# Optimization experiments

Hardware: AMD Instinct MI355X
Metric: run time of the kernel (lower is better)

Reference implementation:

```python
import jax, jax.numpy as jnp
import numpy as np

EMBED = 512
HEADS = 64
DK = EMBED // HEADS  # == n_wires_attn == 8
NW_FFN = 8
FFN = 2048
EPS = 1e-5


def _layernorm(x, g, b):
    mu = jnp.mean(x, axis=-1, keepdims=True)
    var = jnp.var(x, axis=-1, keepdims=True)
    return (x - mu) * jax.lax.rsqrt(var + EPS) * g + b


def setup_inputs() -> dict:
    key = jax.random.key(0)
    ks = jax.random.split(key, 12)
    d = {
        "x": jax.random.normal(ks[0], (4, 1024, EMBED), dtype=jnp.float32),
        # attention quantum RX params (one per wire, shared across heads/tokens)
        "phi": jax.random.normal(ks[1], (DK,), dtype=jnp.float32) * 0.1,
        # combine_heads linear
        "Wc": jax.random.normal(ks[2], (EMBED, EMBED), dtype=jnp.float32) / np.sqrt(EMBED),
        "bc": jnp.zeros((EMBED,), dtype=jnp.float32),
        # FFN quantum RY params
        "theta": jax.random.normal(ks[3], (NW_FFN,), dtype=jnp.float32) * 0.1,
        "W1": jax.random.normal(ks[4], (NW_FFN, FFN), dtype=jnp.float32) / np.sqrt(NW_FFN),
        "b1": jnp.zeros((FFN,), dtype=jnp.float32),
        "W2": jax.random.normal(ks[5], (FFN, EMBED), dtype=jnp.float32) / np.sqrt(FFN),
        "b2": jnp.zeros((EMBED,), dtype=jnp.float32),
        "g1": jnp.ones((EMBED,), dtype=jnp.float32),
        "be1": jnp.zeros((EMBED,), dtype=jnp.float32),
        "g2": jnp.ones((EMBED,), dtype=jnp.float32),
        "be2": jnp.zeros((EMBED,), dtype=jnp.float32),
    }
    return d


def reference(x, phi, Wc, bc, theta, W1, b1, W2, b2, g1, be1, g2, be2):
    B, S, E = x.shape
    # --- quantum attention projections ---
    # Per head-row of DK features: RX(x_i) encoder then trainable RX(phi_i),
    xh = x.reshape(B, S, HEADS, DK)
    qkv = jnp.cos(xh + phi)                     # [B,S,H,DK]
    qkv = jnp.transpose(qkv, (0, 2, 1, 3))      # [B,H,S,DK]
    scores = jnp.einsum('bhqd,bhkd->bhqk', qkv, qkv) / jnp.sqrt(jnp.float32(DK))
    attn = jax.nn.softmax(scores, axis=-1)
    out = jnp.einsum('bhqk,bhkd->bhqd', attn, qkv)
    out = jnp.transpose(out, (0, 2, 1, 3)).reshape(B, S, E)
    attn_out = out @ Wc.T if False else out @ Wc + bc  # combine_heads linear
    x1 = _layernorm(x + attn_out, g1, be1)
    # --- quantum FFN: RX(x_i) then trainable RY(theta_i) -> <Z> = cos(x_i)*cos(theta_i)
    qout = jnp.cos(x1[..., :NW_FFN]) * jnp.cos(theta)   # [B,S,NW_FFN]
    h = jax.nn.relu(qout @ W1 + b1)
    ffn_out = h @ W2 + b2
    return _layernorm(x1 + ffn_out, g2, be2)
```

## Files before the change

kernel.cpp:

```cpp
#include <hip/hip_runtime.h>
#include <hip/hip_bf16.h>
#include <math.h>

#define B 4
#define S 1024
#define E 512
#define H 64
#define DK 8
#define FFN 2048
#define BS (B*S)

#define CSCALE 0.7141879f

#if __has_builtin(__builtin_amdgcn_exp2f)
#define EXP2F(x) __builtin_amdgcn_exp2f(x)
#else
#define EXP2F(x) exp2f(x)
#endif

typedef __attribute__((ext_vector_type(8))) short short8;
typedef __attribute__((ext_vector_type(4))) float float4a;

union U8 { short8 v; unsigned u[4]; };
union F4 { float4a v; float f[4]; };

__device__ __forceinline__ unsigned short f2bf(float f) {
    unsigned u = __builtin_bit_cast(unsigned, f);
    u = (u + 0x7fffu + ((u >> 16) & 1u)) >> 16;
    return (unsigned short)u;
}
__device__ __forceinline__ float bf2f(unsigned short h) {
    return __builtin_bit_cast(float, (unsigned)h << 16);
}
__device__ __forceinline__ unsigned packbf(float a, float b) {
    return __builtin_amdgcn_perm(__builtin_bit_cast(unsigned, a),
                                 __builtin_bit_cast(unsigned, b), 0x07060302u);
}
__device__ __forceinline__ unsigned packbf_rn(float a, float b) {
    return ((unsigned)f2bf(a) << 16) | f2bf(b);
}
__device__ __forceinline__ int pidx(int k) {
    return (k & ~31) | (((k >> 2) & 3) << 3) | (((k >> 4) & 1) << 2) | (k & 3);
}

__device__ __forceinline__ void glds16(const void* g, void* l) {
    __builtin_amdgcn_global_load_lds(
        (const __attribute__((address_space(1))) void*)g,
        (__attribute__((address_space(3))) void*)l, 16, 0, 0);
}

__global__ __launch_bounds__(512) void attn_conv_kernel(const float* __restrict__ x,
                                                        const float* __restrict__ phi,
                                                        const float* __restrict__ Wc,
                                                        const float* __restrict__ W2,
                                                        const float* __restrict__ W1,
                                                        const float* __restrict__ b1,
                                                        unsigned short* __restrict__ Afrag,
                                                        unsigned short* __restrict__ W2f,
                                                        unsigned short* __restrict__ Wcf,
                                                        unsigned short* __restrict__ W1f) {
    __shared__ unsigned short kv[(S + 16) * DK];
    __shared__ unsigned short vtp[9][S + 8];
    int bid = blockIdx.x;
    int tid = threadIdx.x;
    const short8 z8 = {0,0,0,0,0,0,0,0};

    if (bid < 336) {
        int idx = bid * 512 + tid;
        if (idx < 131072) {
            int lane = idx & 63, c = idx >> 6;
            int ntile = c >> 6, kb32 = c & 63;
            int g = lane >> 4, col = lane & 15;
            int n = ntile * 16 + col, kb = kb32 * 32;
            short8 o;
            #pragma unroll
            for (int j = 0; j < 8; j++) {
                int k = kb + 16 * (j >> 2) + 4 * g + (j & 3);
                o[j] = (short)f2bf(W2[(size_t)k * 512 + n]);
            }
            *(short8*)&W2f[(size_t)idx * 8] = o;
        } else if (idx < 163840) {
            int i2 = idx - 131072;
            int lane = i2 & 63, c = i2 >> 6;
            int ntile = c >> 4, kb32 = c & 15;
            int g = lane >> 4, col = lane & 15;
            int n = ntile * 16 + col, kb = kb32 * 32;
            short8 o;
            #pragma unroll
            for (int j = 0; j < 8; j++)
                o[j] = (short)f2bf(Wc[(size_t)(kb + g * 8 + j) * 512 + n]);
            *(short8*)&Wcf[(size_t)i2 * 8] = o;
        } else {
            int i3 = idx - 163840;
            if (i3 < 2048) {
                short8 o;
                #pragma unroll
                for (int j = 0; j < 8; j++) o[j] = (short)f2bf(W1[j * FFN + i3]);
                *(short8*)&W1f[(size_t)i3 * 8] = o;
            } else if (i3 < 4096) {
                int f = i3 - 2048;
                short8 o = z8;
                o[0] = (short)f2bf(b1[f]);
                *(short8*)&W1f[(size_t)i3 * 8] = o;
            } else if (i3 < 4112) {
                *(short8*)&W1f[(size_t)i3 * 8] = z8;
            }
        }
        return;
    }

    int abid = bid - 336;
    int head = abid >> 2, qquad = abid & 3;
    int b = head >> 6, hh = head & 63;

    float ph[DK];
    #pragma unroll
    for (int d = 0; d < DK; d++) ph[d] = phi[d];

    {
        int r2 = tid * 2;
        unsigned short vb[8][2];
        #pragma unroll
        for (int j = 0; j < 2; j++) {
            const float* xp = x + ((size_t)(b * S + r2 + j)) * E + hh * DK;
            float4 u = *(const float4*)xp;
            float4 v = *(const float4*)(xp + 4);
            float c[8] = {__cosf(u.x+ph[0]), __cosf(u.y+ph[1]), __cosf(u.z+ph[2]), __cosf(u.w+ph[3]),
                          __cosf(v.x+ph[4]), __cosf(v.y+ph[5]), __cosf(v.z+ph[6]), __cosf(v.w+ph[7])};
            U8 kr;
            kr.u[0] = packbf_rn(c[1] * CSCALE, c[0] * CSCALE);
            kr.u[1] = packbf_rn(c[3] * CSCALE, c[2] * CSCALE);
            kr.u[2] = packbf_rn(c[5] * CSCALE, c[4] * CSCALE);
            kr.u[3] = packbf_rn(c[7] * CSCALE, c[6] * CSCALE);
            *(short8*)&kv[(r2 + j) * DK] = kr.v;
            #pragma unroll
            for (int d = 0; d < 8; d++) vb[d][j] = f2bf(c[d]);
        }
        int pr = pidx(r2);
        #pragma unroll
        for (int d = 0; d < 8; d++)
            *(unsigned*)&vtp[d][pr] = (unsigned)vb[d][0] | ((unsigned)vb[d][1] << 16);
        *(unsigned*)&vtp[8][pr] = 0x3F803F80u;
    }
    if (tid < 16) *(short8*)&kv[(S + tid) * DK] = z8;
    __syncthreads();

    int w = tid >> 6, lane = tid & 63, col = lane & 15, g = lane >> 4;
    bool g0 = (g == 0);
    int q0 = qquad * 256 + w * 32;
    const float4a zc = {0.f,0.f,0.f,0.f};

    short8 aq[2];
    #pragma unroll
    for (int t = 0; t < 2; t++)
        aq[t] = g0 ? *(const short8*)&kv[(q0 + t*16 + col) * DK] : z8;

    float4a acc[2];
    acc[0] = zc; acc[1] = zc;

    int vrow = col < 8 ? col : 8;
    const unsigned short* vbase = &vtp[vrow][0];

    int off0 = g0 ? col * DK : S * DK;
    int off1 = g0 ? (16 + col) * DK : S * DK;
    int stepo = g0 ? 32 * DK : 0;

    short8 bk0 = *(const short8*)&kv[off0];
    short8 bk1 = *(const short8*)&kv[off1];
    off0 += stepo; off1 += stepo;

    for (int kb = 0; kb < S; kb += 32) {
        __builtin_amdgcn_s_setprio(1);
        float4a s00 = __builtin_amdgcn_mfma_f32_16x16x32_bf16(bk0, aq[0], zc, 0,0,0);
        float4a s01 = __builtin_amdgcn_mfma_f32_16x16x32_bf16(bk1, aq[0], zc, 0,0,0);
        float4a s10 = __builtin_amdgcn_mfma_f32_16x16x32_bf16(bk0, aq[1], zc, 0,0,0);
        float4a s11 = __builtin_amdgcn_mfma_f32_16x16x32_bf16(bk1, aq[1], zc, 0,0,0);
        __builtin_amdgcn_s_setprio(0);
        short8 vf = *(const short8*)(vbase + kb + g * 8);
        short8 nbk0 = *(const short8*)&kv[off0];
        short8 nbk1 = *(const short8*)&kv[off1];
        off0 += stepo; off1 += stepo;
        F4 S00, S01, S10, S11;
        S00.v = s00; S01.v = s01; S10.v = s10; S11.v = s11;
        float ea0 = EXP2F(S00.f[0]);
        float ea1 = EXP2F(S00.f[1]);
        float ea2 = EXP2F(S00.f[2]);
        float ea3 = EXP2F(S00.f[3]);
        float eb0 = EXP2F(S01.f[0]);
        float eb1 = EXP2F(S01.f[1]);
        float eb2 = EXP2F(S01.f[2]);
        float eb3 = EXP2F(S01.f[3]);
        float ec0 = EXP2F(S10.f[0]);
        float ec1 = EXP2F(S10.f[1]);
        float ec2 = EXP2F(S10.f[2]);
        float ec3 = EXP2F(S10.f[3]);
        float ed0 = EXP2F(S11.f[0]);
        float ed1 = EXP2F(S11.f[1]);
        float ed2 = EXP2F(S11.f[2]);
        float ed3 = EXP2F(S11.f[3]);
        U8 pf0, pf1;
        pf0.u[0] = packbf(ea1, ea0);
        pf0.u[1] = packbf(ea3, ea2);
        pf0.u[2] = packbf(eb1, eb0);
        pf0.u[3] = packbf(eb3, eb2);
        pf1.u[0] = packbf(ec1, ec0);
        pf1.u[1] = packbf(ec3, ec2);
        pf1.u[2] = packbf(ed1, ed0);
        pf1.u[3] = packbf(ed3, ed2);
        __builtin_amdgcn_s_setprio(1);
        acc[0] = __builtin_amdgcn_mfma_f32_16x16x32_bf16(vf, pf0.v, acc[0], 0,0,0);
        acc[1] = __builtin_amdgcn_mfma_f32_16x16x32_bf16(vf, pf1.v, acc[1], 0,0,0);
        __builtin_amdgcn_s_setprio(0);
        bk0 = nbk0; bk1 = nbk1;
    }
    int lp8 = ((hh & 3) * 16 + col) * 8;
    #pragma unroll
    for (int t = 0; t < 2; t++) {
        F4 a; a.v = acc[t];
        float denom = __shfl(a.f[0], 32 + col);
        float inv = __builtin_amdgcn_rcpf(denom);
        if (g < 2) {
            int chunk = (hh >> 2) * 256 + (b * 64 + qquad * 16 + w * 2 + t);
            uint2 o;
            o.x = packbf_rn(a.f[1] * inv, a.f[0] * inv);
            o.y = packbf_rn(a.f[3] * inv, a.f[2] * inv);
            *(uint2*)&Afrag[(size_t)chunk * 512 + lp8 + g * 4] = o;
        }
    }
}

__global__ __launch_bounds__(512) void combine_ln1(const unsigned short* __restrict__ Afrag,
                                                   const unsigned short* __restrict__ Wcf,
                                                   const float* __restrict__ bc,
                                                   const float* __restrict__ x,
                                                   const float* __restrict__ g1,
                                                   const float* __restrict__ be1,
                                                   float* __restrict__ x1out,
                                                   unsigned short* __restrict__ qoutbf,
                                                   const float* __restrict__ theta) {
    __shared__ unsigned short As[16 * 64 * 8];
    __shared__ float xout[16][516];
    int tt = blockIdx.x;
    int tid = threadIdx.x;
    int w = tid >> 6, lane = tid & 63;
    int wbase = (tid & ~63) * 8;

    #pragma unroll
    for (int r = 0; r < 2; r++) {
        const unsigned short* gsrc =
            Afrag + ((size_t)((r * 8 + w) * 256 + tt) * 64 + lane) * 8;
        glds16(gsrc, &As[r * 4096 + wbase]);
    }
    asm volatile("s_waitcnt vmcnt(0)" ::: "memory");
    __syncthreads();

    int col = lane & 15, g = lane >> 4;
    const float4a zc = {0.f,0.f,0.f,0.f};
    float4a acc[4];
    #pragma unroll
    for (int nt = 0; nt < 4; nt++) acc[nt] = zc;

    const unsigned short* wp = Wcf + ((size_t)(w * 4096) + lane) * 8;

    short8 bfA[4], bfB[4];
    #pragma unroll
    for (int nt = 0; nt < 4; nt++)
        bfA[nt] = *(const short8*)(wp + nt * 8192);

    for (int kb32 = 0; kb32 < 16; kb32 += 2) {
        #pragma unroll
        for (int nt = 0; nt < 4; nt++)
            bfB[nt] = *(const short8*)(wp + nt * 8192 + (kb32 + 1) * 512);
        short8 af = *(const short8*)&As[(kb32 * 64 + lane) * 8];
        #pragma unroll
        for (int nt = 0; nt < 4; nt++)
            acc[nt] = __builtin_amdgcn_mfma_f32_16x16x32_bf16(af, bfA[nt], acc[nt], 0, 0, 0);
        if (kb32 + 2 < 16) {
            #pragma unroll
            for (int nt = 0; nt < 4; nt++)
                bfA[nt] = *(const short8*)(wp + nt * 8192 + (kb32 + 2) * 512);
        }
        af = *(const short8*)&As[((kb32 + 1) * 64 + lane) * 8];
        #pragma unroll
        for (int nt = 0; nt < 4; nt++)
            acc[nt] = __builtin_amdgcn_mfma_f32_16x16x32_bf16(af, bfB[nt], acc[nt], 0, 0, 0);
    }
    #pragma unroll
    for (int nt = 0; nt < 4; nt++) {
        int n = w * 64 + nt * 16 + col;
        float bb = bc[n];
        #pragma unroll
        for (int r = 0; r < 4; r++)
            xout[g * 4 + r][n] = acc[nt][r] + bb;
    }
    __syncthreads();

    int hl = lane >> 5, l = lane & 31;
    int token = w * 2 + hl;
    int e0 = l * 16;
    size_t grow = ((size_t)tt * 16 + token) * 512;
    float v[16];
    float s = 0.f, sq = 0.f;
    #pragma unroll
    for (int u = 0; u < 4; u++) {
        float4 xv = *(const float4*)&x[grow + e0 + u * 4];
        float4 pv = *(const float4*)&xout[token][e0 + u * 4];
        float a0 = xv.x + pv.x, a1 = xv.y + pv.y, a2 = xv.z + pv.z, a3 = xv.w + pv.w;
        v[u*4] = a0; v[u*4+1] = a1; v[u*4+2] = a2; v[u*4+3] = a3;
        s += a0 + a1 + a2 + a3;
        sq += a0*a0 + a1*a1 + a2*a2 + a3*a3;
    }
    #pragma unroll
    for (int off = 1; off <= 16; off <<= 1) {
        s  += __shfl_xor(s, off);
        sq += __shfl_xor(sq, off);
    }
    float mu = s * (1.f / 512.f);
    float var = sq * (1.f / 512.f) - mu * mu;
    float rstd = rsqrtf(var + 1e-5f);
    float y[16];
    #pragma unroll
    for (int u = 0; u < 4; u++) {
        float4 gv = *(const float4*)&g1[e0 + u * 4];
        float4 bv = *(const float4*)&be1[e0 + u * 4];
        y[u*4]   = (v[u*4]   - mu) * rstd * gv.x + bv.x;
        y[u*4+1] = (v[u*4+1] - mu) * rstd * gv.y + bv.y;
        y[u*4+2] = (v[u*4+2] - mu) * rstd * gv.z + bv.z;
        y[u*4+3] = (v[u*4+3] - mu) * rstd * gv.w + bv.w;
        float4 o = make_float4(y[u*4], y[u*4+1], y[u*4+2], y[u*4+3]);
        *(float4*)&x1out[grow + e0 + u * 4] = o;
    }
    if (l == 0) {
        U8 q;
        q.u[0] = packbf_rn(__cosf(y[1]) * __cosf(theta[1]), __cosf(y[0]) * __cosf(theta[0]));
        q.u[1] = packbf_rn(__cosf(y[3]) * __cosf(theta[3]), __cosf(y[2]) * __cosf(theta[2]));
        q.u[2] = packbf_rn(__cosf(y[5]) * __cosf(theta[5]), __cosf(y[4]) * __cosf(theta[4]));
        q.u[3] = packbf_rn(__cosf(y[7]) * __cosf(theta[7]), __cosf(y[6]) * __cosf(theta[6]));
        *(short8*)&qoutbf[((size_t)tt * 16 + token) * 8] = q.v;
    }
}

__global__ __launch_bounds__(256) void ffn_mfma(const unsigned short* __restrict__ qbf,
                                                const unsigned short* __restrict__ W1fg,
                                                const unsigned short* __restrict__ W2f,
                                                const float* __restrict__ b2,
                                                unsigned short* __restrict__ Cbf) {
    __shared__ float accs[2][64][36];
    int tid = threadIdx.x;
    int w = tid >> 6, lane = tid & 63, col = lane & 15, g = lane >> 4;
    int ngw = w & 1, kh = w >> 1;
    int tb = blockIdx.x >> 2, nb = blockIdx.x & 3;
    int mw = tb * 32;
    int ntile0 = nb * 8 + ngw * 4;
    int kb32b = kh * 32;
    const short8 z8 = {0,0,0,0,0,0,0,0};
    const short8 one8 = {(short)0x3F80,0,0,0,0,0,0,0};
    const float4a zc = {0.f,0.f,0.f,0.f};

    short8 qf[2];
    #pragma unroll
    for (int t = 0; t < 2; t++)
        qf[t] = (g == 0) ? *(const short8*)&qbf[(size_t)(mw + t * 16 + col) * 8]
                         : (g == 1 ? one8 : z8);

    float4a acc[2][4];
    #pragma unroll
    for (int t = 0; t < 2; t++)
        #pragma unroll
        for (int nt = 0; nt < 4; nt++) acc[t][nt] = zc;

    const unsigned short* w2p = W2f + (size_t)ntile0 * 64 * 512 + lane * 8;
    const unsigned short* w1p =
        (g == 0) ? W1fg + (size_t)(kb32b * 32 + col) * 8 :
        (g == 1) ? W1fg + 16384 + (size_t)(kb32b * 32 + col) * 8 :
                   W1fg + 32768;
    int w1step = (g < 2) ? 256 : 0;

    short8 afA[4], afB[4], w1A0, w1A1, w1B0, w1B1;
    #pragma unroll
    for (int nt = 0; nt < 4; nt++)
        afA[nt] = *(const short8*)(w2p + nt * 32768 + (size_t)kb32b * 512);
    w1A0 = *(const short8*)w1p;
    w1A1 = *(const short8*)(w1p + 128);
    w1p += w1step;

#define FFN_BODY(AF, W10, W11)                                                    \
    {                                                                             \
        _Pragma("unroll")                                                         \
        for (int t = 0; t < 2; t++) {                                             \
            float4a h0 = __builtin_amdgcn_mfma_f32_16x16x32_bf16(W10, qf[t], zc, 0,0,0); \
            float4a h1 = __builtin_amdgcn_mfma_f32_16x16x32_bf16(W11, qf[t], zc, 0,0,0); \
            F4 H0, H1; H0.v = h0; H1.v = h1;                                      \
            float e00 = fmaxf(H0.f[0], 0.f);                                      \
            float e01 = fmaxf(H0.f[1], 0.f);                                      \
            float e02 = fmaxf(H0.f[2], 0.f);                                      \
            float e03 = fmaxf(H0.f[3], 0.f);                                      \
            float e10 = fmaxf(H1.f[0], 0.f);                                      \
            float e11 = fmaxf(H1.f[1], 0.f);                                      \
            float e12 = fmaxf(H1.f[2], 0.f);                                      \
            float e13 = fmaxf(H1.f[3], 0.f);                                      \
            U8 pf;                                                                \
            pf.u[0] = packbf(e01, e00);                                           \
            pf.u[1] = packbf(e03, e02);                                           \
            pf.u[2] = packbf(e11, e10);                                           \
            pf.u[3] = packbf(e13, e12);                                           \
            _Pragma("unroll")                                                     \
            for (int nt = 0; nt < 4; nt++)                                        \
                acc[t][nt] = __builtin_amdgcn_mfma_f32_16x16x32_bf16(AF[nt], pf.v, \
                                                                     acc[t][nt], 0,0,0); \
        }                                                                         \
    }

    for (int i = 0; i < 32; i += 2) {
        int kb32 = kb32b + i;
        #pragma unroll
        for (int nt = 0; nt < 4; nt++)
            afB[nt] = *(const short8*)(w2p + nt * 32768 + (size_t)(kb32 + 1) * 512);
        w1B0 = *(const short8*)w1p;
        w1B1 = *(const short8*)(w1p + 128);
        w1p += w1step;
        FFN_BODY(afA, w1A0, w1A1)
        #pragma unroll
        for (int nt = 0; nt < 4; nt++)
            afA[nt] = *(const short8*)(w2p + nt * 32768 + (size_t)(kb32 + 2) * 512);
        w1A0 = *(const short8*)w1p;
        w1A1 = *(const short8*)(w1p + 128);
        w1p += w1step;
        FFN_BODY(afB, w1B0, w1B1)
    }
#undef FFN_BODY

    if (kh == 1) {
        #pragma unroll
        for (int t = 0; t < 2; t++)
            #pragma unroll
            for (int nt = 0; nt < 4; nt++)
                *(float4a*)&accs[ngw][lane][(t * 4 + nt) * 4] = acc[t][nt];
    }
    __syncthreads();
    if (kh == 0) {
        #pragma unroll
        for (int t = 0; t < 2; t++)
            #pragma unroll
            for (int nt = 0; nt < 4; nt++)
                acc[t][nt] = acc[t][nt] +
                    *(const float4a*)&accs[ngw][lane][(t * 4 + nt) * 4];
        int n0 = ntile0 * 16;
        #pragma unroll
        for (int nt = 0; nt < 4; nt++) {
            float4 bb = *(const float4*)&b2[n0 + nt * 16 + 4 * g];
            #pragma unroll
            for (int t = 0; t < 2; t++) {
                F4 a; a.v = acc[t][nt];
                uint2 o;
                o.x = packbf_rn(a.f[1] + bb.y, a.f[0] + bb.x);
                o.y = packbf_rn(a.f[3] + bb.w, a.f[2] + bb.z);
                *(uint2*)&Cbf[(size_t)(mw + t * 16 + col) * 512 + n0 + nt * 16 + 4 * g] = o;
            }
        }
    }
}

__global__ __launch_bounds__(256) void ln_kernel(const float* __restrict__ a,
                                                 const unsigned short* __restrict__ r,
                                                 const float* __restrict__ g,
                                                 const float* __restrict__ be,
                                                 float* __restrict__ out) {
    int t = blockIdx.x * 4 + (threadIdx.x >> 6);
    int lane = threadIdx.x & 63;
    size_t base = (size_t)t * E;
    int e0 = lane * 8;
    float4 a0 = *(const float4*)&a[base + e0];
    float4 a1 = *(const float4*)&a[base + e0 + 4];
    uint4 rv = *(const uint4*)&r[base + e0];
    float v[8];
    v[0] = a0.x + bf2f((unsigned short)(rv.x & 0xffff));
    v[1] = a0.y + bf2f((unsigned short)(rv.x >> 16));
    v[2] = a0.z + bf2f((unsigned short)(rv.y & 0xffff));
    v[3] = a0.w + bf2f((unsigned short)(rv.y >> 16));
    v[4] = a1.x + bf2f((unsigned short)(rv.z & 0xffff));
    v[5] = a1.y + bf2f((unsigned short)(rv.z >> 16));
    v[6] = a1.z + bf2f((unsigned short)(rv.w & 0xffff));
    v[7] = a1.w + bf2f((unsigned short)(rv.w >> 16));
    float s = 0.f, sq = 0.f;
    #pragma unroll
    for (int i = 0; i < 8; i++) { s += v[i]; sq += v[i] * v[i]; }
    #pragma unroll
    for (int off = 1; off <= 32; off <<= 1) {
        s  += __shfl_xor(s, off);
        sq += __shfl_xor(sq, off);
    }
    float mu = s * (1.f / E);
    float var = sq * (1.f / E) - mu * mu;
    float rstd = rsqrtf(var + 1e-5f);
    float4 g0 = *(const float4*)&g[e0];
    float4 g1v = *(const float4*)&g[e0 + 4];
    float4 b0 = *(const float4*)&be[e0];
    float4 b1v = *(const float4*)&be[e0 + 4];
    float4 o0, o1;
    o0.x = (v[0] - mu) * rstd * g0.x + b0.x;
    o0.y = (v[1] - mu) * rstd * g0.y + b0.y;
    o0.z = (v[2] - mu) * rstd * g0.z + b0.z;
    o0.w = (v[3] - mu) * rstd * g0.w + b0.w;
    o1.x = (v[4] - mu) * rstd * g1v.x + b1v.x;
    o1.y = (v[5] - mu) * rstd * g1v.y + b1v.y;
    o1.z = (v[6] - mu) * rstd * g1v.z + b1v.z;
    o1.w = (v[7] - mu) * rstd * g1v.w + b1v.w;
    *(float4*)&out[base + e0] = o0;
    *(float4*)&out[base + e0 + 4] = o1;
}

extern "C" void kernel_launch(void* const* d_in, const int* in_sizes, int n_in,
                              void* d_out, int out_size, void* d_ws, size_t ws_size,
                              hipStream_t stream) {
    const float* x     = (const float*)d_in[0];
    const float* phi   = (const float*)d_in[1];
    const float* Wc    = (const float*)d_in[2];
    const float* bc    = (const float*)d_in[3];
    const float* theta = (const float*)d_in[4];
    const float* W1    = (const float*)d_in[5];
    const float* b1    = (const float*)d_in[6];
    const float* W2    = (const float*)d_in[7];
    const float* b2    = (const float*)d_in[8];
    const float* g1    = (const float*)d_in[9];
    const float* be1   = (const float*)d_in[10];
    const float* g2    = (const float*)d_in[11];
    const float* be2   = (const float*)d_in[12];
    float* out = (float*)d_out;

    float* ws = (float*)d_ws;
    unsigned short* Afrag  = (unsigned short*)ws;
    unsigned short* W2f    = (unsigned short*)(ws + 1048576);
    unsigned short* Wcf    = (unsigned short*)(ws + 1572864);
    unsigned short* W1f    = (unsigned short*)(ws + 1703936);
    unsigned short* qoutbf = (unsigned short*)(ws + 1736704);

    attn_conv_kernel<<<1360, 512, 0, stream>>>(x, phi, Wc, W2, W1, b1,
                                               Afrag, W2f, Wcf, W1f);
    combine_ln1<<<256, 512, 0, stream>>>(Afrag, Wcf, bc, x, g1, be1,
                                         out, qoutbf, theta);
    ffn_mfma<<<512, 256, 0, stream>>>(qoutbf, W1f, W2f, b2, Afrag);
    ln_kernel<<<1024, 256, 0, stream>>>(out, Afrag, g2, be2, out);
}
```

Measured before the change: 155.7 us.

## Fuse FFN second GEMM with final residual LayerNorm in one kernel

Merges the FFN MFMA kernel and the separate LayerNorm kernel. Each 512-thread block now owns 16 full token rows across all 512 output columns with the full K range, and reduces the LayerNorm statistics through shared memory. This drops the bf16 intermediate write and read-back plus one launch, and removes the split-K shared-memory reduction. In exchange the FFN hidden activations for each 16-row tile are recomputed by every wave, W2 is re-streamed once per 16 rows instead of per 32, and the grid shrinks to 256 blocks. The final residual sum also stays in fp32 instead of being rounded to bf16.

Result: slower. 174.5 us (+12.1%).

```diff
diff --git a/kernel.cpp b/kernel.cpp
--- a/kernel.cpp
+++ b/kernel.cpp
@@ -340,79 +340,69 @@
     }
 }
 
-__global__ __launch_bounds__(256) void ffn_mfma(const unsigned short* __restrict__ qbf,
-                                                const unsigned short* __restrict__ W1fg,
-                                                const unsigned short* __restrict__ W2f,
-                                                const float* __restrict__ b2,
-                                                unsigned short* __restrict__ Cbf) {
-    __shared__ float accs[2][64][36];
+__global__ __launch_bounds__(512) void ffn_ln2(const unsigned short* __restrict__ qbf,
+                                               const unsigned short* __restrict__ W1fg,
+                                               const unsigned short* __restrict__ W2f,
+                                               const float* __restrict__ b2,
+                                               const float* __restrict__ g2,
+                                               const float* __restrict__ be2,
+                                               float* __restrict__ out) {
+    __shared__ float sums[8][16], sqs[8][16];
     int tid = threadIdx.x;
     int w = tid >> 6, lane = tid & 63, col = lane & 15, g = lane >> 4;
-    int ngw = w & 1, kh = w >> 1;
-    int tb = blockIdx.x >> 2, nb = blockIdx.x & 3;
-    int mw = tb * 32;
-    int ntile0 = nb * 8 + ngw * 4;
-    int kb32b = kh * 32;
+    int mw = blockIdx.x * 16;
+    int ntile0 = w * 4;
     const short8 z8 = {0,0,0,0,0,0,0,0};
     const short8 one8 = {(short)0x3F80,0,0,0,0,0,0,0};
     const float4a zc = {0.f,0.f,0.f,0.f};
 
-    short8 qf[2];
-    #pragma unroll
-    for (int t = 0; t < 2; t++)
-        qf[t] = (g == 0) ? *(const short8*)&qbf[(size_t)(mw + t * 16 + col) * 8]
+    short8 qf = (g == 0) ? *(const short8*)&qbf[(size_t)(mw + col) * 8]
                          : (g == 1 ? one8 : z8);
 
-    float4a acc[2][4];
-    #pragma unroll
-    for (int t = 0; t < 2; t++)
-        #pragma unroll
-        for (int nt = 0; nt < 4; nt++) acc[t][nt] = zc;
+    float4a acc[4];
+    #pragma unroll
+    for (int nt = 0; nt < 4; nt++) acc[nt] = zc;
 
     const unsigned short* w2p = W2f + (size_t)ntile0 * 64 * 512 + lane * 8;
     const unsigned short* w1p =
-        (g == 0) ? W1fg + (size_t)(kb32b * 32 + col) * 8 :
-        (g == 1) ? W1fg + 16384 + (size_t)(kb32b * 32 + col) * 8 :
+        (g == 0) ? W1fg + (size_t)col * 8 :
+        (g == 1) ? W1fg + 16384 + (size_t)col * 8 :
                    W1fg + 32768;
     int w1step = (g < 2) ? 256 : 0;
 
     short8 afA[4], afB[4], w1A0, w1A1, w1B0, w1B1;
     #pragma unroll
     for (int nt = 0; nt < 4; nt++)
-        afA[nt] = *(const short8*)(w2p + nt * 32768 + (size_t)kb32b * 512);
+        afA[nt] = *(const short8*)(w2p + nt * 32768);
     w1A0 = *(const short8*)w1p;
     w1A1 = *(const short8*)(w1p + 128);
     w1p += w1step;
 
 #define FFN_BODY(AF, W10, W11)                                                    \
     {                                                                             \
+        float4a h0 = __builtin_amdgcn_mfma_f32_16x16x32_bf16(W10, qf, zc, 0,0,0); \
+        float4a h1 = __builtin_amdgcn_mfma_f32_16x16x32_bf16(W11, qf, zc, 0,0,0); \
+        F4 H0, H1; H0.v = h0; H1.v = h1;                                          \
+        float e00 = fmaxf(H0.f[0], 0.f);                                          \
+        float e01 = fmaxf(H0.f[1], 0.f);                                          \
+        float e02 = fmaxf(H0.f[2], 0.f);                                          \
+        float e03 = fmaxf(H0.f[3], 0.f);                                          \
+        float e10 = fmaxf(H1.f[0], 0.f);                                          \
+        float e11 = fmaxf(H1.f[1], 0.f);                                          \
+        float e12 = fmaxf(H1.f[2], 0.f);                                          \
+        float e13 = fmaxf(H1.f[3], 0.f);                                          \
+        U8 pf;                                                                    \
+        pf.u[0] = packbf(e01, e00);                                               \
+        pf.u[1] = packbf(e03, e02);                                               \
+        pf.u[2] = packbf(e11, e10);                                               \
+        pf.u[3] = packbf(e13, e12);                                               \
         _Pragma("unroll")                                                         \
-        for (int t = 0; t < 2; t++) {                                             \
-            float4a h0 = __builtin_amdgcn_mfma_f32_16x16x32_bf16(W10, qf[t], zc, 0,0,0); \
-            float4a h1 = __builtin_amdgcn_mfma_f32_16x16x32_bf16(W11, qf[t], zc, 0,0,0); \
-            F4 H0, H1; H0.v = h0; H1.v = h1;                                      \
-            float e00 = fmaxf(H0.f[0], 0.f);                                      \
-            float e01 = fmaxf(H0.f[1], 0.f);                                      \
-            float e02 = fmaxf(H0.f[2], 0.f);                                      \
-            float e03 = fmaxf(H0.f[3], 0.f);                                      \
-            float e10 = fmaxf(H1.f[0], 0.f);                                      \
-            float e11 = fmaxf(H1.f[1], 0.f);                                      \
-            float e12 = fmaxf(H1.f[2], 0.f);                                      \
-            float e13 = fmaxf(H1.f[3], 0.f);                                      \
-            U8 pf;                                                                \
-            pf.u[0] = packbf(e01, e00);                                           \
-            pf.u[1] = packbf(e03, e02);                                           \
-            pf.u[2] = packbf(e11, e10);                                           \
-            pf.u[3] = packbf(e13, e12);                                           \
-            _Pragma("unroll")                                                     \
-            for (int nt = 0; nt < 4; nt++)                                        \
-                acc[t][nt] = __builtin_amdgcn_mfma_f32_16x16x32_bf16(AF[nt], pf.v, \
-                                                                     acc[t][nt], 0,0,0); \
-        }                                                                         \
-    }
-
-    for (int i = 0; i < 32; i += 2) {
-        int kb32 = kb32b + i;
+        for (int nt = 0; nt < 4; nt++)                                            \
+            acc[nt] = __builtin_amdgcn_mfma_f32_16x16x32_bf16(AF[nt], pf.v,       \
+                                                              acc[nt], 0,0,0);    \
+    }
+
+    for (int kb32 = 0; kb32 < 64; kb32 += 2) {
         #pragma unroll
         for (int nt = 0; nt < 4; nt++)
             afB[nt] = *(const short8*)(w2p + nt * 32768 + (size_t)(kb32 + 1) * 512);
@@ -430,84 +420,45 @@
     }
 #undef FFN_BODY
 
-    if (kh == 1) {
-        #pragma unroll
-        for (int t = 0; t < 2; t++)
-            #pragma unroll
-            for (int nt = 0; nt < 4; nt++)
-                *(float4a*)&accs[ngw][lane][(t * 4 + nt) * 4] = acc[t][nt];
-    }
+    int t = mw + col;
+    size_t base = (size_t)t * E;
+    int nb = w * 64 + 4 * g;
+    float v[16];
+    float s = 0.f, sq = 0.f;
+    #pragma unroll
+    for (int nt = 0; nt < 4; nt++) {
+        float4 bb = *(const float4*)&b2[nb + nt * 16];
+        float4 xv = *(const float4*)&out[base + nb + nt * 16];
+        F4 a; a.v = acc[nt];
+        float v0 = xv.x + a.f[0] + bb.x;
+        float v1 = xv.y + a.f[1] + bb.y;
+        float v2 = xv.z + a.f[2] + bb.z;
+        float v3 = xv.w + a.f[3] + bb.w;
+        v[nt*4] = v0; v[nt*4+1] = v1; v[nt*4+2] = v2; v[nt*4+3] = v3;
+        s += v0 + v1 + v2 + v3;
+        sq += v0*v0 + v1*v1 + v2*v2 + v3*v3;
+    }
+    s  += __shfl_xor(s, 16);  sq += __shfl_xor(sq, 16);
+    s  += __shfl_xor(s, 32);  sq += __shfl_xor(sq, 32);
+    if (lane < 16) { sums[w][col] = s; sqs[w][col] = sq; }
     __syncthreads();
-    if (kh == 0) {
-        #pragma unroll
-        for (int t = 0; t < 2; t++)
-            #pragma unroll
-            for (int nt = 0; nt < 4; nt++)
-                acc[t][nt] = acc[t][nt] +
-                    *(const float4a*)&accs[ngw][lane][(t * 4 + nt) * 4];
-        int n0 = ntile0 * 16;
-        #pragma unroll
-        for (int nt = 0; nt < 4; nt++) {
-            float4 bb = *(const float4*)&b2[n0 + nt * 16 + 4 * g];
-            #pragma unroll
-            for (int t = 0; t < 2; t++) {
-                F4 a; a.v = acc[t][nt];
-                uint2 o;
-                o.x = packbf_rn(a.f[1] + bb.y, a.f[0] + bb.x);
-                o.y = packbf_rn(a.f[3] + bb.w, a.f[2] + bb.z);
-                *(uint2*)&Cbf[(size_t)(mw + t * 16 + col) * 512 + n0 + nt * 16 + 4 * g] = o;
-            }
-        }
-    }
-}
-
-__global__ __launch_bounds__(256) void ln_kernel(const float* __restrict__ a,
-                                                 const unsigned short* __restrict__ r,
-                                                 const float* __restrict__ g,
-                                                 const float* __restrict__ be,
-                                                 float* __restrict__ out) {
-    int t = blockIdx.x * 4 + (threadIdx.x >> 6);
-    int lane = threadIdx.x & 63;
-    size_t base = (size_t)t * E;
-    int e0 = lane * 8;
-    float4 a0 = *(const float4*)&a[base + e0];
-    float4 a1 = *(const float4*)&a[base + e0 + 4];
-    uint4 rv = *(const uint4*)&r[base + e0];
-    float v[8];
-    v[0] = a0.x + bf2f((unsigned short)(rv.x & 0xffff));
-    v[1] = a0.y + bf2f((unsigned short)(rv.x >> 16));
-    v[2] = a0.z + bf2f((unsigned short)(rv.y & 0xffff));
-    v[3] = a0.w + bf2f((unsigned short)(rv.y >> 16));
-    v[4] = a1.x + bf2f((unsigned short)(rv.z & 0xffff));
-    v[5] = a1.y + bf2f((unsigned short)(rv.z >> 16));
-    v[6] = a1.z + bf2f((unsigned short)(rv.w & 0xffff));
-    v[7] = a1.w + bf2f((unsigned short)(rv.w >> 16));
-    float s = 0.f, sq = 0.f;
-    #pragma unroll
-    for (int i = 0; i < 8; i++) { s += v[i]; sq += v[i] * v[i]; }
-    #pragma unroll
-    for (int off = 1; off <= 32; off <<= 1) {
-        s  += __shfl_xor(s, off);
-        sq += __shfl_xor(sq, off);
-    }
-    float mu = s * (1.f / E);
-    float var = sq * (1.f / E) - mu * mu;
+    float SS = 0.f, QQ = 0.f;
+    #pragma unroll
+    for (int ww = 0; ww < 8; ww++) { SS += sums[ww][col]; QQ += sqs[ww][col]; }
+    float mu = SS * (1.f / E);
+    float var = QQ * (1.f / E) - mu * mu;
     float rstd = rsqrtf(var + 1e-5f);
-    float4 g0 = *(const float4*)&g[e0];
-    float4 g1v = *(const float4*)&g[e0 + 4];
-    float4 b0 = *(const float4*)&be[e0];
-    float4 b1v = *(const float4*)&be[e0 + 4];
-    float4 o0, o1;
-    o0.x = (v[0] - mu) * rstd * g0.x + b0.x;
-    o0.y = (v[1] - mu) * rstd * g0.y + b0.y;
-    o0.z = (v[2] - mu) * rstd * g0.z + b0.z;
-    o0.w = (v[3] - mu) * rstd * g0.w + b0.w;
-    o1.x = (v[4] - mu) * rstd * g1v.x + b1v.x;
-    o1.y = (v[5] - mu) * rstd * g1v.y + b1v.y;
-    o1.z = (v[6] - mu) * rstd * g1v.z + b1v.z;
-    o1.w = (v[7] - mu) * rstd * g1v.w + b1v.w;
-    *(float4*)&out[base + e0] = o0;
-    *(float4*)&out[base + e0 + 4] = o1;
+    #pragma unroll
+    for (int nt = 0; nt < 4; nt++) {
+        float4 gv = *(const float4*)&g2[nb + nt * 16];
+        float4 bv = *(const float4*)&be2[nb + nt * 16];
+        float4 o;
+        o.x = (v[nt*4]   - mu) * rstd * gv.x + bv.x;
+        o.y = (v[nt*4+1] - mu) * rstd * gv.y + bv.y;
+        o.z = (v[nt*4+2] - mu) * rstd * gv.z + bv.z;
+        o.w = (v[nt*4+3] - mu) * rstd * gv.w + bv.w;
+        *(float4*)&out[base + nb + nt * 16] = o;
+    }
 }
 
 extern "C" void kernel_launch(void* const* d_in, const int* in_sizes, int n_in,
@@ -539,6 +490,5 @@
                                                Afrag, W2f, Wcf, W1f);
     combine_ln1<<<256, 512, 0, stream>>>(Afrag, Wcf, bc, x, g1, be1,
                                          out, qoutbf, theta);
-    ffn_mfma<<<512, 256, 0, stream>>>(qoutbf, W1f, W2f, b2, Afrag);
-    ln_kernel<<<1024, 256, 0, stream>>>(out, Afrag, g2, be2, out);
-}
+    ffn_ln2<<<256, 512, 0, stream>>>(qoutbf, W1f, W2f, b2, g2, be2, out);
+}
```
